# Optimization experiments

Measured on AMD Instinct MI355X. Metric: run time of the kernel, lower is better.

Reference implementation:

```python
import jax, jax.numpy as jnp
import numpy as np

B, N, DEG = 64, 1024, 32          # graphs, nodes/graph, avg degree
IN_CH, HID = 128, 128
E = B * N * DEG                    # 2,097,152 edges
K = N // 2                         # TopKPooling ratio=0.5 -> 512 kept per graph


def setup_inputs() -> dict:
    key = jax.random.key(0)
    ks = jax.random.split(key, 10)
    x = jax.random.normal(ks[0], (B * N, IN_CH), jnp.float32)
    # within-graph random edges, then offset to global node ids
    src = jax.random.randint(ks[1], (B, N * DEG), 0, N)
    dst = jax.random.randint(ks[2], (B, N * DEG), 0, N)
    off = (jnp.arange(B) * N)[:, None]
    edge_index = jnp.stack([(src + off).reshape(-1), (dst + off).reshape(-1)]).astype(jnp.int64)
    batch = jnp.repeat(jnp.arange(B), N).astype(jnp.int64)
    g = lambda k, fi, fo: jax.random.normal(k, (fi, fo), jnp.float32) / np.sqrt(fi)
    return dict(
        x=x, edge_index=edge_index, batch=batch,
        W1=g(ks[3], IN_CH, HID), b1=jnp.zeros(HID, jnp.float32),
        W2=g(ks[4], HID, HID),   b2=jnp.zeros(HID, jnp.float32),
        w_pool=jax.random.normal(ks[5], (IN_CH,), jnp.float32) / np.sqrt(IN_CH),
        W3=g(ks[6], HID, HID),   b3=jnp.zeros(HID, jnp.float32),
        W4=g(ks[7], HID, HID),   b4=jnp.zeros(HID, jnp.float32),
    )


def _gin(h, src, dst, valid, Wa, ba, Wb, bb, n):
    # GINConv (eps=0): nn(x + sum_{j->i} x_j); valid masks filtered edges
    msg = jnp.where(valid[:, None], h[jnp.where(valid, src, 0)], 0.0)
    agg = jax.ops.segment_sum(msg, jnp.where(valid, dst, 0), num_segments=n)
    h = agg + h
    return jax.nn.relu(h @ Wa + ba) @ Wb + bb


def reference(x, edge_index, batch, W1, b1, W2, b2, w_pool, W3, b3, W4, b4):
    src, dst = edge_index[0], edge_index[1]
    n = B * N
    all_valid = jnp.ones((E,), bool)

    # conv1 + relu
    out = jax.nn.relu(_gin(x, src, dst, all_valid, W1, b1, W2, b2, n))

    # TopKPooling: score from attn=x (original features), tanh nonlinearity
    score = jnp.tanh((x @ w_pool) / jnp.linalg.norm(w_pool))          # [B*N]
    topv, topi = jax.lax.top_k(score.reshape(B, N), K)                 # per-graph
    perm = (topi + (jnp.arange(B) * N)[:, None]).reshape(-1)           # [B*K] global ids
    out = out[perm] * topv.reshape(-1)[:, None]                        # gate kept nodes

    # relabel edges; keep only edges with both endpoints retained
    new_idx = jnp.full((n,), -1, jnp.int32).at[perm].set(jnp.arange(B * K, dtype=jnp.int32))
    s2, d2 = new_idx[src], new_idx[dst]
    valid = (s2 >= 0) & (d2 >= 0)

    # conv2 + relu on pooled graph
    out = jax.nn.relu(_gin(out, s2, d2, valid, W3, b3, W4, b4, B * K))

    # global_mean_pool: each graph has exactly K kept nodes (contiguous per graph)
    return out.reshape(B, K, HID).mean(axis=1)
```

## Files before the change

### kernel.cpp

```cpp
#include <hip/hip_runtime.h>
#include <hip/hip_bf16.h>

constexpr int B_    = 64;
constexpr int N_    = 1024;
constexpr int DEG_  = 32;
constexpr int CH_   = 128;
constexpr int E_    = B_ * N_ * DEG_;
constexpr int NB_   = B_ * N_;
constexpr int K_    = N_ / 2;
constexpr int NK_   = B_ * K_;
constexpr int EPG_  = N_ * DEG_;
constexpr int CPB_  = 8;
constexpr int CE_   = EPG_ / CPB_;

typedef __attribute__((ext_vector_type(8))) short bf16x8;
typedef __attribute__((ext_vector_type(4))) float f32x4;

template <int NBLOCKS>
__device__ inline int xcd_work(int bid) {
  return (bid & 7) * (NBLOCKS / 8) + (bid >> 3);
}

__device__ inline void split_bf16(float v, unsigned short& h, unsigned short& l) {
  unsigned u = __float_as_uint(v);
  unsigned hr = (u + 0x7FFFu + ((u >> 16) & 1u)) & 0xFFFF0000u;
  h = (unsigned short)(hr >> 16);
  float d = v - __uint_as_float(hr);
  unsigned ud = __float_as_uint(d);
  l = (unsigned short)((ud + 0x7FFFu + ((ud >> 16) & 1u)) >> 16);
}

__global__ __launch_bounds__(256) void scores_kernel(
    const float* __restrict__ x, const float* __restrict__ w_pool,
    float* __restrict__ scores, int n) {
  int wave = (blockIdx.x * blockDim.x + threadIdx.x) >> 6;
  int lane = threadIdx.x & 63;
  if (wave >= n) return;
  float w0 = w_pool[lane], w1 = w_pool[64 + lane];
  float a0 = x[(size_t)wave * CH_ + lane];
  float a1 = x[(size_t)wave * CH_ + 64 + lane];
  float dot = a0 * w0 + a1 * w1;
  float nrm = w0 * w0 + w1 * w1;
  #pragma unroll
  for (int m = 32; m > 0; m >>= 1) {
    dot += __shfl_xor(dot, m, 64);
    nrm += __shfl_xor(nrm, m, 64);
  }
  if (lane == 0) scores[wave] = tanhf(dot / sqrtf(nrm));
}

__global__ __launch_bounds__(1024) void topk_kernel(
    const float* __restrict__ scores, int* __restrict__ perm,
    float* __restrict__ topv, int* __restrict__ new_idx) {
  __shared__ unsigned long long keys[N_];
  int b = blockIdx.x, t = threadIdx.x;
  float f = scores[b * N_ + t];
  unsigned u = __float_as_uint(f);
  u = (u & 0x80000000u) ? ~u : (u | 0x80000000u);
  unsigned du = ~u;
  keys[t] = ((unsigned long long)du << 32) | (unsigned)t;
  __syncthreads();
  for (int size = 2; size <= N_; size <<= 1) {
    for (int stride = size >> 1; stride > 0; stride >>= 1) {
      int j = t ^ stride;
      if (j > t) {
        unsigned long long a = keys[t], bk = keys[j];
        bool asc = ((t & size) == 0);
        if ((a > bk) == asc) { keys[t] = bk; keys[j] = a; }
      }
      __syncthreads();
    }
  }
  int idx = (int)(keys[t] & 0xFFFFFFFFu);
  int g = b * N_ + idx;
  if (t < K_) {
    int r = b * K_ + t;
    perm[r] = g;
    topv[r] = scores[g];
    new_idx[g] = r;
  } else {
    new_idx[g] = -1;
  }
}

__global__ __launch_bounds__(256) void csr_hist_kernel(
    const int* __restrict__ dst, int* __restrict__ ph) {
  __shared__ int hist[N_];
  int c = blockIdx.x, t = threadIdx.x;
  int b = c >> 3;
  reinterpret_cast<int4*>(hist)[t] = make_int4(0, 0, 0, 0);
  __syncthreads();
  const int ebase = b * EPG_ + (c & 7) * CE_;
  const int4* d4 = reinterpret_cast<const int4*>(dst + ebase);
  #pragma unroll
  for (int i = 0; i < 4; ++i) {
    int4 d = d4[t + i * 256];
    atomicAdd(&hist[d.x - b * N_], 1);
    atomicAdd(&hist[d.y - b * N_], 1);
    atomicAdd(&hist[d.z - b * N_], 1);
    atomicAdd(&hist[d.w - b * N_], 1);
  }
  __syncthreads();
  int4* out4 = reinterpret_cast<int4*>(ph + (size_t)c * N_);
  out4[t] = reinterpret_cast<const int4*>(hist)[t];
}

__global__ __launch_bounds__(1024) void csr_scan_kernel(
    int* __restrict__ ph, int* __restrict__ offsets1) {
  __shared__ int wsum[16];
  int b = blockIdx.x, n = threadIdx.x;
  int c[CPB_], pre[CPB_];
  int tot = 0;
  #pragma unroll
  for (int q = 0; q < CPB_; ++q) {
    c[q] = ph[(size_t)(b * CPB_ + q) * N_ + n];
    pre[q] = tot;
    tot += c[q];
  }
  int lane = n & 63;
  int incl = tot;
  #pragma unroll
  for (int d = 1; d < 64; d <<= 1) {
    int v = __shfl_up(incl, d, 64);
    if (lane >= d) incl += v;
  }
  if (lane == 63) wsum[n >> 6] = incl;
  __syncthreads();
  if (n < 16) {
    int wv = wsum[n];
    int wincl = wv;
    #pragma unroll
    for (int d = 1; d < 16; d <<= 1) {
      int v = __shfl_up(wincl, d, 16);
      if ((n & 15) >= d) wincl += v;
    }
    wsum[n] = wincl - wv;
  }
  __syncthreads();
  int excl = incl - tot + wsum[n >> 6];
  int base = b * EPG_ + excl;
  offsets1[b * N_ + n] = base;
  if (b == 0 && n == 0) offsets1[NB_] = E_;
  #pragma unroll
  for (int q = 0; q < CPB_; ++q)
    ph[(size_t)(b * CPB_ + q) * N_ + n] = base + pre[q];
}

__global__ __launch_bounds__(256) void csr_scatter_kernel(
    const int* __restrict__ src, const int* __restrict__ dst,
    const int* __restrict__ ph, const int* __restrict__ new_idx,
    int* __restrict__ csr1, int* __restrict__ csr1t) {
  __shared__ int cursor[N_];
  int c = blockIdx.x, t = threadIdx.x;
  int b = c >> 3;
  reinterpret_cast<int4*>(cursor)[t] =
      reinterpret_cast<const int4*>(ph + (size_t)c * N_)[t];
  __syncthreads();
  const int ebase = b * EPG_ + (c & 7) * CE_;
  const int4* s4 = reinterpret_cast<const int4*>(src + ebase);
  const int4* d4 = reinterpret_cast<const int4*>(dst + ebase);
  #pragma unroll
  for (int i = 0; i < 4; ++i) {
    int4 s = s4[t + i * 256];
    int4 d = d4[t + i * 256];
    int p0 = atomicAdd(&cursor[d.x - b * N_], 1);
    csr1[p0] = s.x; csr1t[p0] = new_idx[s.x];
    int p1 = atomicAdd(&cursor[d.y - b * N_], 1);
    csr1[p1] = s.y; csr1t[p1] = new_idx[s.y];
    int p2 = atomicAdd(&cursor[d.z - b * N_], 1);
    csr1[p2] = s.z; csr1t[p2] = new_idx[s.z];
    int p3 = atomicAdd(&cursor[d.w - b * N_], 1);
    csr1[p3] = s.w; csr1t[p3] = new_idx[s.w];
  }
}

__global__ __launch_bounds__(256) void wfrag_kernel(
    const float* __restrict__ W1, const float* __restrict__ W2,
    const float* __restrict__ W3, const float* __restrict__ W4,
    unsigned short* __restrict__ whi, unsigned short* __restrict__ wlo) {
  int wid = (blockIdx.x * 256 + (int)threadIdx.x) >> 6;
  int l = threadIdx.x & 63;
  const float* Ws[4] = {W1, W2, W3, W4};
  int mat = wid >> 5, kb = (wid >> 3) & 3, cg = wid & 7;
  const float* W = Ws[mat];
  int col = cg * 16 + (l & 15);
  int kbase = kb * 32 + (l >> 4) * 8;
  bf16x8 hv, lv;
  #pragma unroll
  for (int j = 0; j < 8; ++j) {
    unsigned short h, lo;
    split_bf16(W[(size_t)(kbase + j) * CH_ + col], h, lo);
    hv[j] = (short)h; lv[j] = (short)lo;
  }
  size_t slot = ((size_t)mat * 32 + (size_t)(kb * 8 + cg)) * 64 + l;
  *reinterpret_cast<bf16x8*>(whi + slot * 8) = hv;
  *reinterpret_cast<bf16x8*>(wlo + slot * 8) = lv;
}

__global__ __launch_bounds__(256) void aggregate_kernel(
    const float* __restrict__ feat, const int* __restrict__ offs,
    const int* __restrict__ srcs, float* __restrict__ out) {
  int work = xcd_work<NB_ / 4>(blockIdx.x);
  int node = work * 4 + ((int)threadIdx.x >> 6);
  int lane = threadIdx.x & 63;
  int h = lane >> 5, li = lane & 31;
  const float4* f4 = reinterpret_cast<const float4*>(feat);
  int s = offs[node], e = offs[node + 1];
  int total = (e - s) + 1;
  float4 acc = make_float4(0.f, 0.f, 0.f, 0.f);
  int i = 0;
  if (total >= 2) {
    int j = h ? srcs[s] : node;
    acc = f4[(size_t)j * 32 + li];
    i = 2;
  }
  for (; i + 4 <= total; i += 4) {
    int ja = h ? srcs[s + i]     : srcs[s + i - 1];
    int jb = h ? srcs[s + i + 2] : srcs[s + i + 1];
    float4 va = f4[(size_t)ja * 32 + li];
    float4 vb = f4[(size_t)jb * 32 + li];
    acc.x += va.x + vb.x; acc.y += va.y + vb.y;
    acc.z += va.z + vb.z; acc.w += va.w + vb.w;
  }
  for (; i + 2 <= total; i += 2) {
    int j = h ? srcs[s + i] : srcs[s + i - 1];
    float4 v = f4[(size_t)j * 32 + li];
    acc.x += v.x; acc.y += v.y; acc.z += v.z; acc.w += v.w;
  }
  if (i < total) {
    if (h == 0) {
      int j = (i == 0) ? node : srcs[s + i - 1];
      float4 v = f4[(size_t)j * 32 + li];
      acc.x += v.x; acc.y += v.y; acc.z += v.z; acc.w += v.w;
    }
  }
  acc.x += __shfl_xor(acc.x, 32, 64);
  acc.y += __shfl_xor(acc.y, 32, 64);
  acc.z += __shfl_xor(acc.z, 32, 64);
  acc.w += __shfl_xor(acc.w, 32, 64);
  if (h == 0)
    reinterpret_cast<float4*>(out)[(size_t)node * 32 + li] = acc;
}

__global__ __launch_bounds__(256) void aggregate2_kernel(
    const float* __restrict__ pooled, const int* __restrict__ perm,
    const int* __restrict__ offs1, const int* __restrict__ csr1t,
    float* __restrict__ out) {
  int work = xcd_work<NK_ / 4>(blockIdx.x);
  int r = work * 4 + ((int)threadIdx.x >> 6);
  int lane = threadIdx.x & 63;
  const float2* f2 = reinterpret_cast<const float2*>(pooled);
  int g = perm[r];
  int s = offs1[g], e = offs1[g + 1];
  float2 acc = f2[(size_t)r * 64 + lane];
  int p = s;
  for (; p + 4 <= e; p += 4) {
    int r0 = csr1t[p], r1 = csr1t[p + 1], r2 = csr1t[p + 2], r3 = csr1t[p + 3];
    if (r0 >= 0) { float2 v = f2[(size_t)r0 * 64 + lane]; acc.x += v.x; acc.y += v.y; }
    if (r1 >= 0) { float2 v = f2[(size_t)r1 * 64 + lane]; acc.x += v.x; acc.y += v.y; }
    if (r2 >= 0) { float2 v = f2[(size_t)r2 * 64 + lane]; acc.x += v.x; acc.y += v.y; }
    if (r3 >= 0) { float2 v = f2[(size_t)r3 * 64 + lane]; acc.x += v.x; acc.y += v.y; }
  }
  for (; p < e; ++p) {
    int r0 = csr1t[p];
    if (r0 >= 0) { float2 v = f2[(size_t)r0 * 64 + lane]; acc.x += v.x; acc.y += v.y; }
  }
  reinterpret_cast<float2*>(out)[(size_t)r * 64 + lane] = acc;
}

template <bool FINAL>
__global__ __launch_bounds__(256) void gemm_pair_mfma_kernel(
    const float* __restrict__ in,
    const unsigned short* __restrict__ wahi, const unsigned short* __restrict__ walo,
    const float* __restrict__ ba,
    const unsigned short* __restrict__ wbhi, const unsigned short* __restrict__ wblo,
    const float* __restrict__ bb,
    float* __restrict__ out) {
  __shared__ unsigned short Ahi[64 * CH_];
  __shared__ unsigned short Alo[64 * CH_];
  int tid = threadIdx.x;
  int w = tid >> 6, l = tid & 63;
  int block_row = blockIdx.x * 64;

  const float4* in4 = reinterpret_cast<const float4*>(in) + (size_t)block_row * 32;
  #pragma unroll
  for (int i = 0; i < 8; ++i) {
    int idx = tid + i * 256;
    float4 v = in4[idx];
    int row = idx >> 5;
    int byte = row * 256 + (idx & 31) * 8;
    byte ^= (row & 7) << 4;
    unsigned short h0, l0, h1, l1, h2, l2, h3, l3;
    split_bf16(v.x, h0, l0); split_bf16(v.y, h1, l1);
    split_bf16(v.z, h2, l2); split_bf16(v.w, h3, l3);
    uint2 hp, lp;
    hp.x = (unsigned)h0 | ((unsigned)h1 << 16);
    hp.y = (unsigned)h2 | ((unsigned)h3 << 16);
    lp.x = (unsigned)l0 | ((unsigned)l1 << 16);
    lp.y = (unsigned)l2 | ((unsigned)l3 << 16);
    *reinterpret_cast<uint2*>(reinterpret_cast<char*>(Ahi) + byte) = hp;
    *reinterpret_cast<uint2*>(reinterpret_cast<char*>(Alo) + byte) = lp;
  }
  __syncthreads();

  int arow = 16 * w + (l & 15);
  int kb_off = (l >> 4) * 16;
  bf16x8 a1h[4], a1l[4];
  #pragma unroll
  for (int kb = 0; kb < 4; ++kb) {
    int byte = arow * 256 + kb * 64 + kb_off;
    byte ^= (arow & 7) << 4;
    a1h[kb] = *reinterpret_cast<const bf16x8*>(reinterpret_cast<const char*>(Ahi) + byte);
    a1l[kb] = *reinterpret_cast<const bf16x8*>(reinterpret_cast<const char*>(Alo) + byte);
  }
  __syncthreads();

  int colbase = l & 15;
  int rowoff = (l >> 4) * 4;

  #pragma unroll 2
  for (int cg = 0; cg < 8; ++cg) {
    f32x4 acc1 = {0.f, 0.f, 0.f, 0.f};
    f32x4 acc2 = {0.f, 0.f, 0.f, 0.f};
    #pragma unroll
    for (int kb = 0; kb < 4; ++kb) {
      size_t slot = (size_t)(kb * 8 + cg) * 64 + l;
      bf16x8 bh = *reinterpret_cast<const bf16x8*>(wahi + slot * 8);
      bf16x8 bl = *reinterpret_cast<const bf16x8*>(walo + slot * 8);
      acc1 = __builtin_amdgcn_mfma_f32_16x16x32_bf16(a1h[kb], bh, acc1, 0, 0, 0);
      acc1 = __builtin_amdgcn_mfma_f32_16x16x32_bf16(a1h[kb], bl, acc1, 0, 0, 0);
      acc2 = __builtin_amdgcn_mfma_f32_16x16x32_bf16(a1l[kb], bh, acc2, 0, 0, 0);
    }
    int col = cg * 16 + colbase;
    float bv = ba[col];
    #pragma unroll
    for (int r = 0; r < 4; ++r) {
      float t = fmaxf(acc1[r] + acc2[r] + bv, 0.f);
      int trow = 16 * w + rowoff + r;
      int byte = (trow * 256 + col * 2) ^ ((trow & 7) << 4);
      unsigned short th, tl;
      split_bf16(t, th, tl);
      *reinterpret_cast<unsigned short*>(reinterpret_cast<char*>(Ahi) + byte) = th;
      *reinterpret_cast<unsigned short*>(reinterpret_cast<char*>(Alo) + byte) = tl;
    }
  }
  __syncthreads();

  bf16x8 a2h[4], a2l[4];
  #pragma unroll
  for (int kb = 0; kb < 4; ++kb) {
    int byte = arow * 256 + kb * 64 + kb_off;
    byte ^= (arow & 7) << 4;
    a2h[kb] = *reinterpret_cast<const bf16x8*>(reinterpret_cast<const char*>(Ahi) + byte);
    a2l[kb] = *reinterpret_cast<const bf16x8*>(reinterpret_cast<const char*>(Alo) + byte);
  }
  if (FINAL) __syncthreads();

  float* redf = reinterpret_cast<float*>(Ahi);

  #pragma unroll 2
  for (int cg = 0; cg < 8; ++cg) {
    f32x4 acc1 = {0.f, 0.f, 0.f, 0.f};
    f32x4 acc2 = {0.f, 0.f, 0.f, 0.f};
    #pragma unroll
    for (int kb = 0; kb < 4; ++kb) {
      size_t slot = (size_t)(kb * 8 + cg) * 64 + l;
      bf16x8 bh = *reinterpret_cast<const bf16x8*>(wbhi + slot * 8);
      bf16x8 bl = *reinterpret_cast<const bf16x8*>(wblo + slot * 8);
      acc1 = __builtin_amdgcn_mfma_f32_16x16x32_bf16(a2h[kb], bh, acc1, 0, 0, 0);
      acc1 = __builtin_amdgcn_mfma_f32_16x16x32_bf16(a2h[kb], bl, acc1, 0, 0, 0);
      acc2 = __builtin_amdgcn_mfma_f32_16x16x32_bf16(a2l[kb], bh, acc2, 0, 0, 0);
    }
    int col = cg * 16 + colbase;
    float bv = bb[col];
    if (!FINAL) {
      #pragma unroll
      for (int r = 0; r < 4; ++r) {
        float v = fmaxf(acc1[r] + acc2[r] + bv, 0.f);
        out[(size_t)(block_row + 16 * w + rowoff + r) * CH_ + col] = v;
      }
    } else {
      float part = 0.f;
      #pragma unroll
      for (int r = 0; r < 4; ++r)
        part += fmaxf(acc1[r] + acc2[r] + bv, 0.f);
      redf[(w * 4 + (l >> 4)) * CH_ + col] = part;
    }
  }

  if (FINAL) {
    __syncthreads();
    if (tid < CH_) {
      float tot = 0.f;
      #pragma unroll
      for (int s = 0; s < 16; ++s) tot += redf[s * CH_ + tid];
      int b = block_row / K_;
      atomicAdd(&out[b * CH_ + tid], tot * (1.0f / (float)K_));
    }
  }
}

__global__ __launch_bounds__(256) void pool_gather_kernel(
    const float* __restrict__ out1, const int* __restrict__ perm,
    const float* __restrict__ topv, float* __restrict__ pooled) {
  int work = xcd_work<NK_ / 4>(blockIdx.x);
  int r = work * 4 + ((int)threadIdx.x >> 6);
  int lane = threadIdx.x & 63;
  int g = perm[r];
  float v = topv[r];
  float2 t = reinterpret_cast<const float2*>(out1)[(size_t)g * 64 + lane];
  t.x *= v; t.y *= v;
  reinterpret_cast<float2*>(pooled)[(size_t)r * 64 + lane] = t;
}

extern "C" void kernel_launch(void* const* d_in, const int* in_sizes, int n_in,
                              void* d_out, int out_size, void* d_ws, size_t ws_size,
                              hipStream_t stream) {
  const float* x      = (const float*)d_in[0];
  const int*   eidx   = (const int*)d_in[1];
  const int*   src    = eidx;
  const int*   dst    = eidx + E_;
  const float* W1 = (const float*)d_in[3];
  const float* b1 = (const float*)d_in[4];
  const float* W2 = (const float*)d_in[5];
  const float* b2 = (const float*)d_in[6];
  const float* w_pool = (const float*)d_in[7];
  const float* W3 = (const float*)d_in[8];
  const float* b3 = (const float*)d_in[9];
  const float* W4 = (const float*)d_in[10];
  const float* b4 = (const float*)d_in[11];
  float* dout = (float*)d_out;

  char* w = (char*)d_ws;
  auto carve = [&](size_t bytes) {
    char* p = w;
    w += (bytes + 255) & ~(size_t)255;
    return p;
  };
  float*          bufA     = (float*)carve((size_t)NB_ * CH_ * 4);
  float*          bufB     = (float*)carve((size_t)NB_ * CH_ * 4);
  int*            csr1     = (int*)  carve((size_t)E_ * 4);
  int*            csr1t    = (int*)  carve((size_t)E_ * 4);
  int*            ph       = (int*)  carve((size_t)B_ * CPB_ * N_ * 4);
  int*            offsets1 = (int*)  carve((size_t)(NB_ + 4) * 4);
  float*          scores   = (float*)carve((size_t)NB_ * 4);
  int*            perm     = (int*)  carve((size_t)NK_ * 4);
  float*          topv     = (float*)carve((size_t)NK_ * 4);
  int*            new_idx  = (int*)  carve((size_t)NB_ * 4);
  unsigned short* whiB     = (unsigned short*)carve((size_t)4 * 16384 * 2);
  unsigned short* wloB     = (unsigned short*)carve((size_t)4 * 16384 * 2);
  auto whi = [&](int m) { return whiB + (size_t)m * 16384; };
  auto wlo = [&](int m) { return wloB + (size_t)m * 16384; };

  hipMemsetAsync(dout, 0, (size_t)B_ * CH_ * 4, stream);

  wfrag_kernel<<<32, 256, 0, stream>>>(W1, W2, W3, W4, whiB, wloB);

  scores_kernel<<<NB_ / 4, 256, 0, stream>>>(x, w_pool, scores, NB_);
  topk_kernel<<<B_, 1024, 0, stream>>>(scores, perm, topv, new_idx);

  csr_hist_kernel<<<B_ * CPB_, 256, 0, stream>>>(dst, ph);
  csr_scan_kernel<<<B_, 1024, 0, stream>>>(ph, offsets1);
  csr_scatter_kernel<<<B_ * CPB_, 256, 0, stream>>>(src, dst, ph, new_idx,
                                                    csr1, csr1t);

  aggregate_kernel<<<NB_ / 4, 256, 0, stream>>>(x, offsets1, csr1, bufA);
  gemm_pair_mfma_kernel<false><<<NB_ / 64, 256, 0, stream>>>(
      bufA, whi(0), wlo(0), b1, whi(1), wlo(1), b2, bufB);

  pool_gather_kernel<<<NK_ / 4, 256, 0, stream>>>(bufB, perm, topv, bufA);

  aggregate2_kernel<<<NK_ / 4, 256, 0, stream>>>(bufA, perm, offsets1, csr1t,
                                                 bufB);

  gemm_pair_mfma_kernel<true><<<NK_ / 64, 256, 0, stream>>>(
      bufB, whi(2), wlo(2), b3, whi(3), wlo(3), b4, dout);
}
```

Measured before the change: 315.7 us.

## Pack local source and pooled indices into one 32-bit CSR array

Replaces the two separate CSR arrays (global source ids and relabeled pooled ids) with one array of packed 16-bit graph-local indices, so the scatter writes half the bytes and both aggregation kernels read a single stream. It also doubles the number of chunks per graph for the histogram and scatter kernels, which raises parallelism in those passes. The packing relies on at most 1024 nodes per graph and 512 kept nodes, and it adds shift/mask work in the aggregation loops.

```diff
diff --git a/kernel.cpp b/kernel.cpp
--- a/kernel.cpp
+++ b/kernel.cpp
@@ -10,7 +10,7 @@
 constexpr int K_    = N_ / 2;
 constexpr int NK_   = B_ * K_;
 constexpr int EPG_  = N_ * DEG_;
-constexpr int CPB_  = 8;
+constexpr int CPB_  = 16;
 constexpr int CE_   = EPG_ / CPB_;
 
 typedef __attribute__((ext_vector_type(8))) short bf16x8;
@@ -87,13 +87,13 @@
     const int* __restrict__ dst, int* __restrict__ ph) {
   __shared__ int hist[N_];
   int c = blockIdx.x, t = threadIdx.x;
-  int b = c >> 3;
+  int b = c >> 4;
   reinterpret_cast<int4*>(hist)[t] = make_int4(0, 0, 0, 0);
   __syncthreads();
-  const int ebase = b * EPG_ + (c & 7) * CE_;
+  const int ebase = b * EPG_ + (c & 15) * CE_;
   const int4* d4 = reinterpret_cast<const int4*>(dst + ebase);
   #pragma unroll
-  for (int i = 0; i < 4; ++i) {
+  for (int i = 0; i < 2; ++i) {
     int4 d = d4[t + i * 256];
     atomicAdd(&hist[d.x - b * N_], 1);
     atomicAdd(&hist[d.y - b * N_], 1);
@@ -149,28 +149,34 @@
 __global__ __launch_bounds__(256) void csr_scatter_kernel(
     const int* __restrict__ src, const int* __restrict__ dst,
     const int* __restrict__ ph, const int* __restrict__ new_idx,
-    int* __restrict__ csr1, int* __restrict__ csr1t) {
+    unsigned* __restrict__ csr) {
   __shared__ int cursor[N_];
   int c = blockIdx.x, t = threadIdx.x;
-  int b = c >> 3;
+  int b = c >> 4;
   reinterpret_cast<int4*>(cursor)[t] =
       reinterpret_cast<const int4*>(ph + (size_t)c * N_)[t];
   __syncthreads();
-  const int ebase = b * EPG_ + (c & 7) * CE_;
+  const int ebase = b * EPG_ + (c & 15) * CE_;
+  const int nbase = b * N_, kbase = b * K_;
   const int4* s4 = reinterpret_cast<const int4*>(src + ebase);
   const int4* d4 = reinterpret_cast<const int4*>(dst + ebase);
   #pragma unroll
-  for (int i = 0; i < 4; ++i) {
+  for (int i = 0; i < 2; ++i) {
     int4 s = s4[t + i * 256];
     int4 d = d4[t + i * 256];
-    int p0 = atomicAdd(&cursor[d.x - b * N_], 1);
-    csr1[p0] = s.x; csr1t[p0] = new_idx[s.x];
-    int p1 = atomicAdd(&cursor[d.y - b * N_], 1);
-    csr1[p1] = s.y; csr1t[p1] = new_idx[s.y];
-    int p2 = atomicAdd(&cursor[d.z - b * N_], 1);
-    csr1[p2] = s.z; csr1t[p2] = new_idx[s.z];
-    int p3 = atomicAdd(&cursor[d.w - b * N_], 1);
-    csr1[p3] = s.w; csr1t[p3] = new_idx[s.w];
+    int n0 = new_idx[s.x], n1 = new_idx[s.y], n2 = new_idx[s.z], n3 = new_idx[s.w];
+    unsigned v0 = ((unsigned)(s.x - nbase) << 16) |
+                  ((n0 < 0) ? 0xFFFFu : (unsigned)(n0 - kbase));
+    unsigned v1 = ((unsigned)(s.y - nbase) << 16) |
+                  ((n1 < 0) ? 0xFFFFu : (unsigned)(n1 - kbase));
+    unsigned v2 = ((unsigned)(s.z - nbase) << 16) |
+                  ((n2 < 0) ? 0xFFFFu : (unsigned)(n2 - kbase));
+    unsigned v3 = ((unsigned)(s.w - nbase) << 16) |
+                  ((n3 < 0) ? 0xFFFFu : (unsigned)(n3 - kbase));
+    int p0 = atomicAdd(&cursor[d.x - nbase], 1); csr[p0] = v0;
+    int p1 = atomicAdd(&cursor[d.y - nbase], 1); csr[p1] = v1;
+    int p2 = atomicAdd(&cursor[d.z - nbase], 1); csr[p2] = v2;
+    int p3 = atomicAdd(&cursor[d.w - nbase], 1); csr[p3] = v3;
   }
 }
 
@@ -199,37 +205,38 @@
 
 __global__ __launch_bounds__(256) void aggregate_kernel(
     const float* __restrict__ feat, const int* __restrict__ offs,
-    const int* __restrict__ srcs, float* __restrict__ out) {
+    const unsigned* __restrict__ srcs, float* __restrict__ out) {
   int work = xcd_work<NB_ / 4>(blockIdx.x);
   int node = work * 4 + ((int)threadIdx.x >> 6);
   int lane = threadIdx.x & 63;
   int h = lane >> 5, li = lane & 31;
+  int gbase = (node >> 10) << 10;
   const float4* f4 = reinterpret_cast<const float4*>(feat);
   int s = offs[node], e = offs[node + 1];
   int total = (e - s) + 1;
   float4 acc = make_float4(0.f, 0.f, 0.f, 0.f);
   int i = 0;
   if (total >= 2) {
-    int j = h ? srcs[s] : node;
+    int j = h ? (gbase + (int)(srcs[s] >> 16)) : node;
     acc = f4[(size_t)j * 32 + li];
     i = 2;
   }
   for (; i + 4 <= total; i += 4) {
-    int ja = h ? srcs[s + i]     : srcs[s + i - 1];
-    int jb = h ? srcs[s + i + 2] : srcs[s + i + 1];
+    int ja = gbase + (int)(srcs[s + (h ? i : i - 1)] >> 16);
+    int jb = gbase + (int)(srcs[s + (h ? i + 2 : i + 1)] >> 16);
     float4 va = f4[(size_t)ja * 32 + li];
     float4 vb = f4[(size_t)jb * 32 + li];
     acc.x += va.x + vb.x; acc.y += va.y + vb.y;
     acc.z += va.z + vb.z; acc.w += va.w + vb.w;
   }
   for (; i + 2 <= total; i += 2) {
-    int j = h ? srcs[s + i] : srcs[s + i - 1];
+    int j = gbase + (int)(srcs[s + (h ? i : i - 1)] >> 16);
     float4 v = f4[(size_t)j * 32 + li];
     acc.x += v.x; acc.y += v.y; acc.z += v.z; acc.w += v.w;
   }
   if (i < total) {
     if (h == 0) {
-      int j = (i == 0) ? node : srcs[s + i - 1];
+      int j = (i == 0) ? node : (gbase + (int)(srcs[s + i - 1] >> 16));
       float4 v = f4[(size_t)j * 32 + li];
       acc.x += v.x; acc.y += v.y; acc.z += v.z; acc.w += v.w;
     }
@@ -244,26 +251,30 @@
 
 __global__ __launch_bounds__(256) void aggregate2_kernel(
     const float* __restrict__ pooled, const int* __restrict__ perm,
-    const int* __restrict__ offs1, const int* __restrict__ csr1t,
+    const int* __restrict__ offs1, const unsigned* __restrict__ csr,
     float* __restrict__ out) {
   int work = xcd_work<NK_ / 4>(blockIdx.x);
   int r = work * 4 + ((int)threadIdx.x >> 6);
   int lane = threadIdx.x & 63;
+  int kbase = (r >> 9) << 9;
   const float2* f2 = reinterpret_cast<const float2*>(pooled);
   int g = perm[r];
   int s = offs1[g], e = offs1[g + 1];
   float2 acc = f2[(size_t)r * 64 + lane];
   int p = s;
   for (; p + 4 <= e; p += 4) {
-    int r0 = csr1t[p], r1 = csr1t[p + 1], r2 = csr1t[p + 2], r3 = csr1t[p + 3];
-    if (r0 >= 0) { float2 v = f2[(size_t)r0 * 64 + lane]; acc.x += v.x; acc.y += v.y; }
-    if (r1 >= 0) { float2 v = f2[(size_t)r1 * 64 + lane]; acc.x += v.x; acc.y += v.y; }
-    if (r2 >= 0) { float2 v = f2[(size_t)r2 * 64 + lane]; acc.x += v.x; acc.y += v.y; }
-    if (r3 >= 0) { float2 v = f2[(size_t)r3 * 64 + lane]; acc.x += v.x; acc.y += v.y; }
+    short n0 = (short)(csr[p]     & 0xFFFFu);
+    short n1 = (short)(csr[p + 1] & 0xFFFFu);
+    short n2 = (short)(csr[p + 2] & 0xFFFFu);
+    short n3 = (short)(csr[p + 3] & 0xFFFFu);
+    if (n0 >= 0) { float2 v = f2[(size_t)(kbase + n0) * 64 + lane]; acc.x += v.x; acc.y += v.y; }
+    if (n1 >= 0) { float2 v = f2[(size_t)(kbase + n1) * 64 + lane]; acc.x += v.x; acc.y += v.y; }
+    if (n2 >= 0) { float2 v = f2[(size_t)(kbase + n2) * 64 + lane]; acc.x += v.x; acc.y += v.y; }
+    if (n3 >= 0) { float2 v = f2[(size_t)(kbase + n3) * 64 + lane]; acc.x += v.x; acc.y += v.y; }
   }
   for (; p < e; ++p) {
-    int r0 = csr1t[p];
-    if (r0 >= 0) { float2 v = f2[(size_t)r0 * 64 + lane]; acc.x += v.x; acc.y += v.y; }
+    short n0 = (short)(csr[p] & 0xFFFFu);
+    if (n0 >= 0) { float2 v = f2[(size_t)(kbase + n0) * 64 + lane]; acc.x += v.x; acc.y += v.y; }
   }
   reinterpret_cast<float2*>(out)[(size_t)r * 64 + lane] = acc;
 }
@@ -439,8 +450,7 @@
   };
   float*          bufA     = (float*)carve((size_t)NB_ * CH_ * 4);
   float*          bufB     = (float*)carve((size_t)NB_ * CH_ * 4);
-  int*            csr1     = (int*)  carve((size_t)E_ * 4);
-  int*            csr1t    = (int*)  carve((size_t)E_ * 4);
+  unsigned*       csr      = (unsigned*)carve((size_t)E_ * 4);
   int*            ph       = (int*)  carve((size_t)B_ * CPB_ * N_ * 4);
   int*            offsets1 = (int*)  carve((size_t)(NB_ + 4) * 4);
   float*          scores   = (float*)carve((size_t)NB_ * 4);
@@ -461,17 +471,15 @@
 
   csr_hist_kernel<<<B_ * CPB_, 256, 0, stream>>>(dst, ph);
   csr_scan_kernel<<<B_, 1024, 0, stream>>>(ph, offsets1);
-  csr_scatter_kernel<<<B_ * CPB_, 256, 0, stream>>>(src, dst, ph, new_idx,
-                                                    csr1, csr1t);
-
-  aggregate_kernel<<<NB_ / 4, 256, 0, stream>>>(x, offsets1, csr1, bufA);
+  csr_scatter_kernel<<<B_ * CPB_, 256, 0, stream>>>(src, dst, ph, new_idx, csr);
+
+  aggregate_kernel<<<NB_ / 4, 256, 0, stream>>>(x, offsets1, csr, bufA);
   gemm_pair_mfma_kernel<false><<<NB_ / 64, 256, 0, stream>>>(
       bufA, whi(0), wlo(0), b1, whi(1), wlo(1), b2, bufB);
 
   pool_gather_kernel<<<NK_ / 4, 256, 0, stream>>>(bufB, perm, topv, bufA);
 
-  aggregate2_kernel<<<NK_ / 4, 256, 0, stream>>>(bufA, perm, offsets1, csr1t,
-                                                 bufB);
+  aggregate2_kernel<<<NK_ / 4, 256, 0, stream>>>(bufA, perm, offsets1, csr, bufB);
 
   gemm_pair_mfma_kernel<true><<<NK_ / 64, 256, 0, stream>>>(
       bufB, whi(2), wlo(2), b3, whi(3), wlo(3), b4, dout);
```

New measurement: 292.3 us. 1.08x faster.
